# Optimization experiments

Hardware: AMD Instinct MI355X
Metric: run time of the kernel (lower is better)

## Reference

```python
import jax, jax.numpy as jnp
import numpy as np

N_NODES = 100000
N_EDGES = 1600000
IN_DIM, HID_DIM, OUT_DIM = 128, 64, 32
NEG_SLOPE = 0.2  # PyG GATConv default negative_slope


def gat_conv(x, src, dst, num_nodes, W, a_src, a_dst, bias):
    # x: [N, in], W: [in, out], a_src/a_dst: [out], bias: [out]
    h = x @ W                                        # [N, out]
    alpha_s = h @ a_src                              # [N] per-node source score
    alpha_d = h @ a_dst                              # [N] per-node target score
    e = jax.nn.leaky_relu(alpha_s[src] + alpha_d[dst], NEG_SLOPE)  # [E]
    # segment softmax over incoming edges of each dst node
    m = jax.ops.segment_max(e, dst, num_segments=num_nodes)        # [N]
    ex = jnp.exp(e - m[dst])                                        # [E]
    z = jax.ops.segment_sum(ex, dst, num_segments=num_nodes)        # [N]
    coef = ex / z[dst]                                              # [E]
    out = jax.ops.segment_sum(coef[:, None] * h[src], dst, num_segments=num_nodes)
    return out + bias


def setup_inputs() -> dict:
    key = jax.random.key(0)
    ks = jax.random.split(key, 10)
    x = jax.random.normal(ks[0], (N_NODES, IN_DIM), dtype=jnp.float32)
    edge_index = jax.random.randint(ks[1], (2, N_EDGES), 0, N_NODES, dtype=jnp.int64)
    s = 0.1
    W1 = jax.random.normal(ks[2], (IN_DIM, HID_DIM), dtype=jnp.float32) * s
    a_src1 = jax.random.normal(ks[3], (HID_DIM,), dtype=jnp.float32) * s
    a_dst1 = jax.random.normal(ks[4], (HID_DIM,), dtype=jnp.float32) * s
    b1 = jnp.zeros((HID_DIM,), dtype=jnp.float32)
    W2 = jax.random.normal(ks[5], (HID_DIM, OUT_DIM), dtype=jnp.float32) * s
    a_src2 = jax.random.normal(ks[6], (OUT_DIM,), dtype=jnp.float32) * s
    a_dst2 = jax.random.normal(ks[7], (OUT_DIM,), dtype=jnp.float32) * s
    b2 = jnp.zeros((OUT_DIM,), dtype=jnp.float32)
    return {"x": x, "edge_index": edge_index, "W1": W1, "a_src1": a_src1,
            "a_dst1": a_dst1, "b1": b1, "W2": W2, "a_src2": a_src2,
            "a_dst2": a_dst2, "b2": b2}


def reference(x, edge_index, W1, a_src1, a_dst1, b1, W2, a_src2, a_dst2, b2):
    n = x.shape[0]
    loops = jnp.arange(n, dtype=edge_index.dtype)
    src = jnp.concatenate([edge_index[0], loops])  # add_self_loops=True default
    dst = jnp.concatenate([edge_index[1], loops])
    h = jax.nn.relu(gat_conv(x, src, dst, n, W1, a_src1, a_dst1, b1))
    out = gat_conv(h, src, dst, n, W2, a_src2, a_dst2, b2)
    return jax.nn.log_softmax(out, axis=1)
```

## Files before the change

kernel.cpp:

```cpp
#include <hip/hip_runtime.h>

#define N_NODES 100000
#define N_EDGES 1600000
#define ET (N_EDGES + N_NODES)
#define NEG_SLOPE 0.2f

#define BSHIFT 9
#define BW 512
#define NBUCK ((N_NODES + BW - 1) / BW)
#define BCAP 10240
#define BINCH 2048

typedef unsigned short u16;
typedef unsigned int u32;

__device__ __forceinline__ float bf2f(u16 v) {
    return __uint_as_float(((u32)v) << 16);
}
__device__ __forceinline__ u16 f2bf(float f) {
    u32 u = __float_as_uint(f);
    u32 r = (u + 0x7FFFu + ((u >> 16) & 1u)) >> 16;
    return (u16)r;
}
__device__ __forceinline__ float lrelu(float x) { return x > 0.f ? x : NEG_SLOPE * x; }
__device__ __forceinline__ float ldf(const void* p, int i, int bf) {
    return bf ? bf2f(((const u16*)p)[i]) : ((const float*)p)[i];
}
__device__ __forceinline__ int get_dst(const int* __restrict__ ei, int e, int ei64) {
    if (e < N_EDGES) return ei64 ? ei[2 * (N_EDGES + e)] : ei[N_EDGES + e];
    return e - N_EDGES;
}
__device__ __forceinline__ int get_src(const int* __restrict__ ei, int e, int ei64) {
    if (e < N_EDGES) return ei64 ? ei[2 * e] : ei[e];
    return e - N_EDGES;
}

__device__ __forceinline__ void fma8(float wt, uint4 qv, float (&acc)[8]) {
    acc[0] = fmaf(wt, __uint_as_float(qv.x << 16), acc[0]);
    acc[1] = fmaf(wt, __uint_as_float(qv.x & 0xFFFF0000u), acc[1]);
    acc[2] = fmaf(wt, __uint_as_float(qv.y << 16), acc[2]);
    acc[3] = fmaf(wt, __uint_as_float(qv.y & 0xFFFF0000u), acc[3]);
    acc[4] = fmaf(wt, __uint_as_float(qv.z << 16), acc[4]);
    acc[5] = fmaf(wt, __uint_as_float(qv.z & 0xFFFF0000u), acc[5]);
    acc[6] = fmaf(wt, __uint_as_float(qv.w << 16), acc[6]);
    acc[7] = fmaf(wt, __uint_as_float(qv.w & 0xFFFF0000u), acc[7]);
}

__global__ void detect_kernel(const u32* __restrict__ x32, const int* __restrict__ ei,
                              int* __restrict__ flags, int* __restrict__ bcnt) {
    int lane = threadIdx.x;
    for (int i = lane; i < 256; i += 64) bcnt[i] = 0;
    u32 e = (x32[lane] >> 7) & 0xFFu;
    int ok = (e >= 96u && e <= 143u) ? 1 : 0;
    int cnt = (int)__popcll(__ballot(ok));
    int nz = (ei[2 * lane + 1] != 0) + (ei[2 * (lane + 64) + 1] != 0);
    #pragma unroll
    for (int off = 32; off > 0; off >>= 1) nz += __shfl_xor(nz, off);
    if (lane == 0) { flags[0] = (cnt >= 48) ? 1 : 0; flags[1] = (nz == 0) ? 1 : 0; }
}

__global__ __launch_bounds__(256) void bin_kernel(
    const int* __restrict__ ei, const int* __restrict__ flags,
    int* __restrict__ bcnt, u32* __restrict__ bbuf)
{
    __shared__ int hist[NBUCK];
    const int t = threadIdx.x;
    const int base = blockIdx.x * BINCH;
    const int ei64 = flags[1];
    for (int i = t; i < NBUCK; i += 256) hist[i] = 0;
    __syncthreads();
    for (int i = t; i < BINCH; i += 256) {
        int e = base + i;
        if (e >= ET) break;
        int d = get_dst(ei, e, ei64);
        atomicAdd(&hist[d >> BSHIFT], 1);
    }
    __syncthreads();
    for (int i = t; i < NBUCK; i += 256) {
        int c = hist[i];
        hist[i] = (c > 0) ? atomicAdd(&bcnt[i], c) : 0;
    }
    __syncthreads();
    for (int i = t; i < BINCH; i += 256) {
        int e = base + i;
        if (e >= ET) break;
        int d = get_dst(ei, e, ei64);
        int s = get_src(ei, e, ei64);
        int b = d >> BSHIFT;
        int pos = atomicAdd(&hist[b], 1);
        if (pos < BCAP)
            bbuf[(size_t)b * BCAP + pos] = ((u32)(d & (BW - 1)) << 17) | (u32)s;
    }
}

__global__ __launch_bounds__(256) void bscan_kernel(
    const int* __restrict__ bcnt, int* __restrict__ bbase)
{
    __shared__ int sd[256];
    int t = threadIdx.x;
    int v = (t < NBUCK) ? min(bcnt[t], BCAP) : 0;
    sd[t] = v;
    __syncthreads();
    for (int off = 1; off < 256; off <<= 1) {
        int x = (t >= off) ? sd[t - off] : 0;
        __syncthreads();
        sd[t] += x;
        __syncthreads();
    }
    if (t < NBUCK) bbase[t] = sd[t] - v;
    if (t == NBUCK - 1) bbase[NBUCK] = sd[t];
}

__global__ __launch_bounds__(1024) void scatter_kernel(
    const int* __restrict__ bcnt, const int* __restrict__ bbase,
    const u32* __restrict__ bbuf, int* __restrict__ rowptr, int* __restrict__ ssrc)
{
    __shared__ int hist[BW];
    __shared__ int cur[BW];
    __shared__ int wtot[4];
    __shared__ int lds_s[BCAP];
    const int t = threadIdx.x;
    const int b = blockIdx.x;
    const int cnt = min(bcnt[b], BCAP);
    const int base = bbase[b];
    const u32* mybuf = bbuf + (size_t)b * BCAP;

    if (t < BW) hist[t] = 0;
    __syncthreads();
    for (int i = t; i < cnt; i += 1024) atomicAdd(&hist[(int)(mybuf[i] >> 17)], 1);
    __syncthreads();
    int a0 = 0, a1 = 0, s = 0, v = 0;
    const int lane = t & 63, wid = t >> 6;
    if (t < 256) {
        a0 = hist[2 * t]; a1 = hist[2 * t + 1];
        s = a0 + a1;
        v = s;
        #pragma unroll
        for (int off = 1; off < 64; off <<= 1) {
            int n = __shfl_up(v, off);
            if (lane >= off) v += n;
        }
        if (lane == 63) wtot[wid] = v;
    }
    __syncthreads();
    if (t == 0) {
        int acc = 0;
        #pragma unroll
        for (int w = 0; w < 4; ++w) { int tmp = wtot[w]; wtot[w] = acc; acc += tmp; }
    }
    __syncthreads();
    if (t < 256) {
        int excl = v + wtot[wid] - s;
        cur[2 * t] = excl;
        cur[2 * t + 1] = excl + a0;
    }
    __syncthreads();
    if (t < BW) {
        int g = b * BW + t;
        if (g < N_NODES) rowptr[g] = base + cur[t];
    }
    if (b == NBUCK - 1 && t == 0) rowptr[N_NODES] = bbase[NBUCK];
    __syncthreads();
    for (int i = t; i < cnt; i += 1024) {
        u32 code = mybuf[i];
        int pos = atomicAdd(&cur[(int)(code >> 17)], 1);
        lds_s[pos] = (int)(code & 0x1FFFFu);
    }
    __syncthreads();
    for (int i = t; i < cnt; i += 1024) ssrc[base + i] = lds_s[i];
}

__global__ __launch_bounds__(256) void gemm1_kernel(
    const float* __restrict__ x, const float* __restrict__ W,
    const void* __restrict__ a_src, const void* __restrict__ a_dst,
    const int* __restrict__ flags,
    u16* __restrict__ h, float* __restrict__ as_, float* __restrict__ ad_)
{
    __shared__ float xs[256 * 33];
    __shared__ float Wl[32 * 64];
    const int t = threadIdx.x;
    const int node0 = blockIdx.x * 256;
    const int bf = flags[0];
    const int ng = t >> 3;
    const int cg = t & 7;

    float acc[8][8];
    #pragma unroll
    for (int i = 0; i < 8; ++i)
        #pragma unroll
        for (int j = 0; j < 8; ++j) acc[i][j] = 0.f;

    for (int kc = 0; kc < 4; ++kc) {
        const int kb = kc * 32;
        const int c4 = t & 7;
        #pragma unroll
        for (int p = 0; p < 8; ++p) {
            int row = (t >> 3) + p * 32;
            int n = node0 + row;
            float4 vv = make_float4(0.f, 0.f, 0.f, 0.f);
            if (n < N_NODES) {
                if (!bf) {
                    vv = *(const float4*)(x + (size_t)n * 128 + kb + c4 * 4);
                } else {
                    const u16* xh = (const u16*)x;
                    vv.x = bf2f(xh[(size_t)n * 128 + kb + c4 * 4 + 0]);
                    vv.y = bf2f(xh[(size_t)n * 128 + kb + c4 * 4 + 1]);
                    vv.z = bf2f(xh[(size_t)n * 128 + kb + c4 * 4 + 2]);
                    vv.w = bf2f(xh[(size_t)n * 128 + kb + c4 * 4 + 3]);
                }
            }
            float* dstp = &xs[row * 33 + c4 * 4];
            dstp[0] = vv.x; dstp[1] = vv.y; dstp[2] = vv.z; dstp[3] = vv.w;
        }
        if (!bf) {
            #pragma unroll
            for (int qq = 0; qq < 2; ++qq) {
                int f4 = t * 2 + qq;
                ((float4*)Wl)[f4] = ((const float4*)(W + (size_t)kb * 64))[f4];
            }
        } else {
            const u16* Wh = (const u16*)W;
            for (int i = t; i < 2048; i += 256) Wl[i] = bf2f(Wh[(size_t)kb * 64 + i]);
        }
        __syncthreads();

        for (int kk = 0; kk < 32; ++kk) {
            float xr[8];
            #pragma unroll
            for (int i = 0; i < 8; ++i) xr[i] = xs[(ng * 8 + i) * 33 + kk];
            float4 w0 = *(const float4*)&Wl[kk * 64 + cg * 8];
            float4 w1 = *(const float4*)&Wl[kk * 64 + cg * 8 + 4];
            const float wr[8] = {w0.x, w0.y, w0.z, w0.w, w1.x, w1.y, w1.z, w1.w};
            #pragma unroll
            for (int i = 0; i < 8; ++i)
                #pragma unroll
                for (int j = 0; j < 8; ++j)
                    acc[i][j] = fmaf(xr[i], wr[j], acc[i][j]);
        }
        __syncthreads();
    }

    float av[8], dv[8];
    #pragma unroll
    for (int j = 0; j < 8; ++j) {
        av[j] = ldf(a_src, cg * 8 + j, bf);
        dv[j] = ldf(a_dst, cg * 8 + j, bf);
    }
    #pragma unroll
    for (int i = 0; i < 8; ++i) {
        int n = node0 + ng * 8 + i;
        float ps = 0.f, pd = 0.f;
        #pragma unroll
        for (int j = 0; j < 8; ++j) { ps += acc[i][j] * av[j]; pd += acc[i][j] * dv[j]; }
        #pragma unroll
        for (int off = 1; off < 8; off <<= 1) {
            ps += __shfl_xor(ps, off);
            pd += __shfl_xor(pd, off);
        }
        if (n < N_NODES) {
            uint4 hv;
            hv.x = (u32)f2bf(acc[i][0]) | ((u32)f2bf(acc[i][1]) << 16);
            hv.y = (u32)f2bf(acc[i][2]) | ((u32)f2bf(acc[i][3]) << 16);
            hv.z = (u32)f2bf(acc[i][4]) | ((u32)f2bf(acc[i][5]) << 16);
            hv.w = (u32)f2bf(acc[i][6]) | ((u32)f2bf(acc[i][7]) << 16);
            *(uint4*)&h[(size_t)n * 64 + cg * 8] = hv;
            if (cg == 0) { as_[n] = ps; ad_[n] = pd; }
        }
    }
}

template<int SH>
__global__ __launch_bounds__(256) void score_kernel(
    const int* __restrict__ rowptr, const int* __restrict__ ssrc,
    const float* __restrict__ as_, const float* __restrict__ ad_,
    uint2* __restrict__ wexs)
{
    const int lane = threadIdx.x & 63;
    const int dst = blockIdx.x * 4 + (threadIdx.x >> 6);
    if (dst >= N_NODES) return;
    const int beg = rowptr[dst], end = rowptr[dst + 1];
    const int deg = end - beg;
    const float add = ad_[dst];

    if (deg <= 64) {
        int j = beg + lane;
        bool valid = j < end;
        int sj = valid ? ssrc[j] : 0;
        float sc = valid ? lrelu(as_[sj] + add) : -1e30f;
        float m = sc;
        #pragma unroll
        for (int off = 32; off > 0; off >>= 1) m = fmaxf(m, __shfl_xor(m, off));
        float ex = __expf(sc - m);
        float l = ex;
        #pragma unroll
        for (int off = 32; off > 0; off >>= 1) l += __shfl_xor(l, off);
        if (valid)
            wexs[j] = make_uint2(__float_as_uint(ex / l), ((u32)sj) << SH);
    } else {
        float m = -1e30f, l = 0.f;
        for (int base = beg; base < end; base += 64) {
            int j = base + lane;
            bool valid = j < end;
            float sc = valid ? lrelu(as_[ssrc[j]] + add) : -1e30f;
            float cm = sc;
            #pragma unroll
            for (int off = 32; off > 0; off >>= 1) cm = fmaxf(cm, __shfl_xor(cm, off));
            float nm = fmaxf(m, cm);
            float cs = __expf(sc - nm);
            #pragma unroll
            for (int off = 32; off > 0; off >>= 1) cs += __shfl_xor(cs, off);
            l = l * __expf(m - nm) + cs;
            m = nm;
        }
        float inv = 1.f / l;
        for (int base = beg; base < end; base += 64) {
            int j = base + lane;
            if (j < end) {
                int sj = ssrc[j];
                wexs[j] = make_uint2(
                    __float_as_uint(__expf(lrelu(as_[sj] + add) - m) * inv),
                    ((u32)sj) << SH);
            }
        }
    }
}

__global__ __launch_bounds__(256) void gather64_kernel(
    const int* __restrict__ rowptr, const uint2* __restrict__ wexs,
    const u16* __restrict__ h, float* __restrict__ agg)
{
    const int tid = threadIdx.x;
    const int hl = tid & 31;
    const int dreal = blockIdx.x * 8 + (tid >> 5);
    const int dst = min(dreal, N_NODES - 1);
    const int beg = rowptr[dst];
    const int deg = rowptr[dst + 1] - beg;
    const int e4 = hl >> 3;
    const int i8 = hl & 7;
    const char* __restrict__ hb = (const char*)h;
    const u32 boff = (u32)(i8 * 16);

    float acc[8] = {0.f, 0.f, 0.f, 0.f, 0.f, 0.f, 0.f, 0.f};

    #pragma unroll
    for (int g = 0; g < 8; ++g) {
        int eidx = g * 4 + e4;
        bool valid = eidx < deg;
        uint2 p = wexs[beg + (valid ? eidx : 0)];
        float w = valid ? __uint_as_float(p.x) : 0.f;
        uint4 qv = *(const uint4*)(hb + (size_t)(p.y + boff));
        fma8(w, qv, acc);
    }
    int mdeg = max(deg, __shfl_xor(deg, 32));
    for (int g = 8; g * 4 < mdeg; ++g) {
        int eidx = g * 4 + e4;
        bool valid = eidx < deg;
        uint2 p = wexs[beg + (valid ? eidx : 0)];
        float w = valid ? __uint_as_float(p.x) : 0.f;
        uint4 qv = *(const uint4*)(hb + (size_t)(p.y + boff));
        fma8(w, qv, acc);
    }

    #pragma unroll
    for (int c = 0; c < 8; ++c) {
        acc[c] += __shfl_xor(acc[c], 8);
        acc[c] += __shfl_xor(acc[c], 16);
    }
    if (e4 == 0 && dreal < N_NODES) {
        *(float4*)&agg[(size_t)dst * 64 + i8 * 8] =
            make_float4(acc[0], acc[1], acc[2], acc[3]);
        *(float4*)&agg[(size_t)dst * 64 + i8 * 8 + 4] =
            make_float4(acc[4], acc[5], acc[6], acc[7]);
    }
}

__global__ __launch_bounds__(256) void gather32_lsm_kernel(
    const int* __restrict__ rowptr, const uint2* __restrict__ wexs,
    const u16* __restrict__ h, const void* __restrict__ b2,
    const int* __restrict__ flags, float* __restrict__ out)
{
    const int tid = threadIdx.x;
    const int hl = tid & 31;
    const int dreal = blockIdx.x * 8 + (tid >> 5);
    const int dst = min(dreal, N_NODES - 1);
    const int beg = rowptr[dst];
    const int deg = rowptr[dst + 1] - beg;
    const int e8 = hl >> 2;
    const int i4 = hl & 3;
    const int bf = flags[0];
    const char* __restrict__ hb = (const char*)h;
    const u32 boff = (u32)(i4 * 16);

    float acc[8] = {0.f, 0.f, 0.f, 0.f, 0.f, 0.f, 0.f, 0.f};

    #pragma unroll
    for (int g = 0; g < 4; ++g) {
        int eidx = g * 8 + e8;
        bool valid = eidx < deg;
        uint2 p = wexs[beg + (valid ? eidx : 0)];
        float w = valid ? __uint_as_float(p.x) : 0.f;
        uint4 qv = *(const uint4*)(hb + (size_t)(p.y + boff));
        fma8(w, qv, acc);
    }
    int mdeg = max(deg, __shfl_xor(deg, 32));
    for (int g = 4; g * 8 < mdeg; ++g) {
        int eidx = g * 8 + e8;
        bool valid = eidx < deg;
        uint2 p = wexs[beg + (valid ? eidx : 0)];
        float w = valid ? __uint_as_float(p.x) : 0.f;
        uint4 qv = *(const uint4*)(hb + (size_t)(p.y + boff));
        fma8(w, qv, acc);
    }

    #pragma unroll
    for (int c = 0; c < 8; ++c) {
        acc[c] += __shfl_xor(acc[c], 4);
        acc[c] += __shfl_xor(acc[c], 8);
        acc[c] += __shfl_xor(acc[c], 16);
    }

    float v[8];
    #pragma unroll
    for (int c = 0; c < 8; ++c) v[c] = acc[c] + ldf(b2, i4 * 8 + c, bf);
    float mx = v[0];
    #pragma unroll
    for (int c = 1; c < 8; ++c) mx = fmaxf(mx, v[c]);
    mx = fmaxf(mx, __shfl_xor(mx, 1));
    mx = fmaxf(mx, __shfl_xor(mx, 2));
    float ss = 0.f;
    #pragma unroll
    for (int c = 0; c < 8; ++c) ss += __expf(v[c] - mx);
    ss += __shfl_xor(ss, 1);
    ss += __shfl_xor(ss, 2);
    float lg = mx + __logf(ss);
    if (e8 == 0 && dreal < N_NODES) {
        *(float4*)&out[(size_t)dst * 32 + i4 * 8] =
            make_float4(v[0] - lg, v[1] - lg, v[2] - lg, v[3] - lg);
        *(float4*)&out[(size_t)dst * 32 + i4 * 8 + 4] =
            make_float4(v[4] - lg, v[5] - lg, v[6] - lg, v[7] - lg);
    }
}

#define G2_TILE 128

__global__ __launch_bounds__(256, 3) void gemm2_kernel(
    const float* __restrict__ agg1, const void* __restrict__ b1,
    const u32* __restrict__ W32, const void* __restrict__ a_src,
    const void* __restrict__ a_dst, const int* __restrict__ flags,
    u16* __restrict__ h, float* __restrict__ as_, float* __restrict__ ad_)
{
    __shared__ __align__(16) float Wl[64 * 32];
    __shared__ __align__(16) float xs[G2_TILE * 68];
    const int tid = threadIdx.x;
    const int node0 = blockIdx.x * G2_TILE;
    const int bf = flags[0];

    if (bf) {
        for (int i = tid; i < 1024; i += 256) {
            u32 u = W32[i];
            *(float2*)&Wl[2 * i] = make_float2(__uint_as_float(u << 16),
                                               __uint_as_float(u & 0xFFFF0000u));
        }
    } else {
        for (int i = tid; i < 2048; i += 256) Wl[i] = __uint_as_float(W32[i]);
    }
    #pragma unroll
    for (int it = 0; it < 8; ++it) {
        int i = tid + it * 256;
        int nl = i >> 4;
        int k  = (i & 15) * 4;
        int n = node0 + nl;
        float4 v = make_float4(0.f, 0.f, 0.f, 0.f);
        if (n < N_NODES) v = *(const float4*)(agg1 + (size_t)n * 64 + k);
        v.x = fmaxf(v.x + ldf(b1, k + 0, bf), 0.f);
        v.y = fmaxf(v.y + ldf(b1, k + 1, bf), 0.f);
        v.z = fmaxf(v.z + ldf(b1, k + 2, bf), 0.f);
        v.w = fmaxf(v.w + ldf(b1, k + 3, bf), 0.f);
        *(float4*)&xs[nl * 68 + k] = v;
    }
    __syncthreads();

    const int ch0 = (tid & 7) * 4;
    const int nb0 = (tid >> 3) * 4;
    float acc[4][4];
    #pragma unroll
    for (int j = 0; j < 4; ++j)
        #pragma unroll
        for (int c = 0; c < 4; ++c) acc[j][c] = 0.f;

    #pragma unroll 4
    for (int k0 = 0; k0 < 64; k0 += 4) {
        float4 xv0 = *(const float4*)&xs[(nb0 + 0) * 68 + k0];
        float4 xv1 = *(const float4*)&xs[(nb0 + 1) * 68 + k0];
        float4 xv2 = *(const float4*)&xs[(nb0 + 2) * 68 + k0];
        float4 xv3 = *(const float4*)&xs[(nb0 + 3) * 68 + k0];
        const float* xp[4] = { (const float*)&xv0, (const float*)&xv1,
                               (const float*)&xv2, (const float*)&xv3 };
        #pragma unroll
        for (int kk = 0; kk < 4; ++kk) {
            float4 w = *(const float4*)&Wl[(k0 + kk) * 32 + ch0];
            #pragma unroll
            for (int j = 0; j < 4; ++j) {
                float xvv = xp[j][kk];
                acc[j][0] = fmaf(xvv, w.x, acc[j][0]);
                acc[j][1] = fmaf(xvv, w.y, acc[j][1]);
                acc[j][2] = fmaf(xvv, w.z, acc[j][2]);
                acc[j][3] = fmaf(xvv, w.w, acc[j][3]);
            }
        }
    }

    float av[4], dv[4];
    #pragma unroll
    for (int c = 0; c < 4; ++c) {
        av[c] = ldf(a_src, ch0 + c, bf);
        dv[c] = ldf(a_dst, ch0 + c, bf);
    }
    #pragma unroll
    for (int j = 0; j < 4; ++j) {
        float ps = acc[j][0] * av[0] + acc[j][1] * av[1]
                 + acc[j][2] * av[2] + acc[j][3] * av[3];
        float pd = acc[j][0] * dv[0] + acc[j][1] * dv[1]
                 + acc[j][2] * dv[2] + acc[j][3] * dv[3];
        #pragma unroll
        for (int off = 1; off < 8; off <<= 1) {
            ps += __shfl_xor(ps, off);
            pd += __shfl_xor(pd, off);
        }
        int n = node0 + nb0 + j;
        if (n < N_NODES) {
            u32 p0 = (u32)f2bf(acc[j][0]) | ((u32)f2bf(acc[j][1]) << 16);
            u32 p1 = (u32)f2bf(acc[j][2]) | ((u32)f2bf(acc[j][3]) << 16);
            *(uint2*)&h[(size_t)n * 32 + ch0] = make_uint2(p0, p1);
            if ((tid & 7) == 0) { as_[n] = ps; ad_[n] = pd; }
        }
    }
}

extern "C" void kernel_launch(void* const* d_in, const int* in_sizes, int n_in,
                              void* d_out, int out_size, void* d_ws, size_t ws_size,
                              hipStream_t stream) {
    const float* x   = (const float*)d_in[0];
    const int* ei    = (const int*)d_in[1];
    const float* W1  = (const float*)d_in[2];
    const void* a_s1 = d_in[3];
    const void* a_d1 = d_in[4];
    const void* b1   = d_in[5];
    const u32* W2    = (const u32*)d_in[6];
    const void* a_s2 = d_in[7];
    const void* a_d2 = d_in[8];
    const void* b2   = d_in[9];
    float* out = (float*)d_out;

    char* base = (char*)d_ws;
    int* flags = (int*)base;
    u16* h     = (u16*)(base + 64);
    char* q = base + 64 + (size_t)N_NODES * 64 * 2;
    float* as1 = (float*)q; q += (size_t)N_NODES * 4;
    float* ad1 = (float*)q; q += (size_t)N_NODES * 4;
    float* as2 = (float*)q; q += (size_t)N_NODES * 4;
    float* ad2 = (float*)q; q += (size_t)N_NODES * 4;
    float* agg1 = (float*)q; q += (size_t)N_NODES * 64 * 4;
    int* rowptr = (int*)q;  q += (size_t)(N_NODES + 16) * 4;
    int* ssrc   = (int*)q;  q += (size_t)ET * 4;
    int* bcnt   = (int*)q;  q += 256 * 4;
    int* bbase  = (int*)q;  q += 256 * 4;
    q = (char*)(((size_t)q + 255) & ~(size_t)255);
    u32*  bbuf  = (u32*)q;
    uint2* wexs = (uint2*)q;

    detect_kernel<<<1, 64, 0, stream>>>((const u32*)x, ei, flags, bcnt);

    bin_kernel<<<(ET + BINCH - 1) / BINCH, 256, 0, stream>>>(ei, flags, bcnt, bbuf);
    bscan_kernel<<<1, 256, 0, stream>>>(bcnt, bbase);
    scatter_kernel<<<NBUCK, 1024, 0, stream>>>(bcnt, bbase, bbuf, rowptr, ssrc);

    gemm1_kernel<<<(N_NODES + 255) / 256, 256, 0, stream>>>(x, W1, a_s1, a_d1, flags, h, as1, ad1);
    score_kernel<7><<<(N_NODES + 3) / 4, 256, 0, stream>>>(rowptr, ssrc, as1, ad1, wexs);
    gather64_kernel<<<(N_NODES + 7) / 8, 256, 0, stream>>>(rowptr, wexs, h, agg1);

    gemm2_kernel<<<(N_NODES + G2_TILE - 1) / G2_TILE, 256, 0, stream>>>(agg1, b1, W2, a_s2, a_d2, flags, h, as2, ad2);
    score_kernel<6><<<(N_NODES + 3) / 4, 256, 0, stream>>>(rowptr, ssrc, as2, ad2, wexs);
    gather32_lsm_kernel<<<(N_NODES + 7) / 8, 256, 0, stream>>>(rowptr, wexs, h, b2, flags, out);
}
```

Before: 338.4 us.

## Fuse layer-2 GEMM into layer-1 gather and cache edges in registers during binning

Removes the separate gemm2 kernel and the fp32 agg1 round trip. Each wave now applies bias and ReLU to its aggregated 64-wide row, multiplies it by a transposed W2 held in LDS, computes the attention scores and writes bf16 h2 directly. Layer-2 output goes to a new h2 buffer instead of overwriting h. Separately, bin_kernel keeps each thread's edge src/dst in registers between its histogram and scatter passes instead of reading the edge list twice. The trade-off is that every gather block reloads and transposes all of W2 into LDS, adding per-block setup work and LDS use.

```diff
diff --git a/kernel.cpp b/kernel.cpp
--- a/kernel.cpp
+++ b/kernel.cpp
@@ -69,11 +69,18 @@
     const int ei64 = flags[1];
     for (int i = t; i < NBUCK; i += 256) hist[i] = 0;
     __syncthreads();
-    for (int i = t; i < BINCH; i += 256) {
-        int e = base + i;
-        if (e >= ET) break;
-        int d = get_dst(ei, e, ei64);
-        atomicAdd(&hist[d >> BSHIFT], 1);
+
+    int dloc[8], sloc[8];
+    #pragma unroll
+    for (int p = 0; p < 8; ++p) {
+        int e = base + t + p * 256;
+        if (e < ET) {
+            dloc[p] = get_dst(ei, e, ei64);
+            sloc[p] = get_src(ei, e, ei64);
+            atomicAdd(&hist[dloc[p] >> BSHIFT], 1);
+        } else {
+            dloc[p] = -1; sloc[p] = 0;
+        }
     }
     __syncthreads();
     for (int i = t; i < NBUCK; i += 256) {
@@ -81,15 +88,15 @@
         hist[i] = (c > 0) ? atomicAdd(&bcnt[i], c) : 0;
     }
     __syncthreads();
-    for (int i = t; i < BINCH; i += 256) {
-        int e = base + i;
-        if (e >= ET) break;
-        int d = get_dst(ei, e, ei64);
-        int s = get_src(ei, e, ei64);
-        int b = d >> BSHIFT;
-        int pos = atomicAdd(&hist[b], 1);
-        if (pos < BCAP)
-            bbuf[(size_t)b * BCAP + pos] = ((u32)(d & (BW - 1)) << 17) | (u32)s;
+    #pragma unroll
+    for (int p = 0; p < 8; ++p) {
+        if (dloc[p] >= 0) {
+            int b = dloc[p] >> BSHIFT;
+            int pos = atomicAdd(&hist[b], 1);
+            if (pos < BCAP)
+                bbuf[(size_t)b * BCAP + pos] =
+                    ((u32)(dloc[p] & (BW - 1)) << 17) | (u32)sloc[p];
+        }
     }
 }
 
@@ -325,14 +332,37 @@
     }
 }
 
-__global__ __launch_bounds__(256) void gather64_kernel(
+__global__ __launch_bounds__(256) void gather64_g2_kernel(
     const int* __restrict__ rowptr, const uint2* __restrict__ wexs,
-    const u16* __restrict__ h, float* __restrict__ agg)
-{
+    const u16* __restrict__ h, const void* __restrict__ b1,
+    const u32* __restrict__ W32, const void* __restrict__ a_src,
+    const void* __restrict__ a_dst, const int* __restrict__ flags,
+    u16* __restrict__ h2, float* __restrict__ as2, float* __restrict__ ad2)
+{
+    __shared__ float W2t[32 * 66];
+    __shared__ float hin_lds[8 * 64];
     const int tid = threadIdx.x;
     const int hl = tid & 31;
     const int dreal = blockIdx.x * 8 + (tid >> 5);
     const int dst = min(dreal, N_NODES - 1);
+    const int bf = flags[0];
+
+    if (bf) {
+        for (int i = tid; i < 1024; i += 256) {
+            u32 u = W32[i];
+            int k = i >> 4;
+            int c = (2 * i) & 31;
+            W2t[c * 66 + k] = __uint_as_float(u << 16);
+            W2t[(c + 1) * 66 + k] = __uint_as_float(u & 0xFFFF0000u);
+        }
+    } else {
+        for (int i = tid; i < 2048; i += 256) {
+            int k = i >> 5, c = i & 31;
+            W2t[c * 66 + k] = __uint_as_float(W32[i]);
+        }
+    }
+    __syncthreads();
+
     const int beg = rowptr[dst];
     const int deg = rowptr[dst + 1] - beg;
     const int e4 = hl >> 3;
@@ -366,12 +396,48 @@
         acc[c] += __shfl_xor(acc[c], 8);
         acc[c] += __shfl_xor(acc[c], 16);
     }
-    if (e4 == 0 && dreal < N_NODES) {
-        *(float4*)&agg[(size_t)dst * 64 + i8 * 8] =
-            make_float4(acc[0], acc[1], acc[2], acc[3]);
-        *(float4*)&agg[(size_t)dst * 64 + i8 * 8 + 4] =
-            make_float4(acc[4], acc[5], acc[6], acc[7]);
-    }
+
+    float* hin_s = &hin_lds[(tid >> 5) * 64];
+    if (hl < 8) {
+        float4 v0, v1;
+        v0.x = fmaxf(acc[0] + ldf(b1, hl * 8 + 0, bf), 0.f);
+        v0.y = fmaxf(acc[1] + ldf(b1, hl * 8 + 1, bf), 0.f);
+        v0.z = fmaxf(acc[2] + ldf(b1, hl * 8 + 2, bf), 0.f);
+        v0.w = fmaxf(acc[3] + ldf(b1, hl * 8 + 3, bf), 0.f);
+        v1.x = fmaxf(acc[4] + ldf(b1, hl * 8 + 4, bf), 0.f);
+        v1.y = fmaxf(acc[5] + ldf(b1, hl * 8 + 5, bf), 0.f);
+        v1.z = fmaxf(acc[6] + ldf(b1, hl * 8 + 6, bf), 0.f);
+        v1.w = fmaxf(acc[7] + ldf(b1, hl * 8 + 7, bf), 0.f);
+        *(float4*)&hin_s[hl * 8] = v0;
+        *(float4*)&hin_s[hl * 8 + 4] = v1;
+    }
+    __builtin_amdgcn_wave_barrier();
+    asm volatile("s_waitcnt lgkmcnt(0)" ::: "memory");
+
+    float o = 0.f;
+    #pragma unroll 8
+    for (int k = 0; k < 64; k += 2) {
+        float2 hv = *(const float2*)&hin_s[k];
+        float2 wv = *(const float2*)&W2t[hl * 66 + k];
+        o = fmaf(hv.x, wv.x, o);
+        o = fmaf(hv.y, wv.y, o);
+    }
+
+    float ps = o * ldf(a_src, hl, bf);
+    float pd = o * ldf(a_dst, hl, bf);
+    #pragma unroll
+    for (int off = 1; off < 32; off <<= 1) {
+        ps += __shfl_xor(ps, off);
+        pd += __shfl_xor(pd, off);
+    }
+    u32 hbits = (u32)f2bf(o);
+    u32 other = (u32)__shfl_xor((int)hbits, 1);
+    if (dreal < N_NODES) {
+        if ((hl & 1) == 0)
+            *((u32*)h2 + (size_t)dst * 16 + (hl >> 1)) = hbits | (other << 16);
+        if (hl == 0) { as2[dst] = ps; ad2[dst] = pd; }
+    }
+    __builtin_amdgcn_wave_barrier();
 }
 
 __global__ __launch_bounds__(256) void gather32_lsm_kernel(
@@ -438,102 +504,6 @@
             make_float4(v[0] - lg, v[1] - lg, v[2] - lg, v[3] - lg);
         *(float4*)&out[(size_t)dst * 32 + i4 * 8 + 4] =
             make_float4(v[4] - lg, v[5] - lg, v[6] - lg, v[7] - lg);
-    }
-}
-
-#define G2_TILE 128
-
-__global__ __launch_bounds__(256, 3) void gemm2_kernel(
-    const float* __restrict__ agg1, const void* __restrict__ b1,
-    const u32* __restrict__ W32, const void* __restrict__ a_src,
-    const void* __restrict__ a_dst, const int* __restrict__ flags,
-    u16* __restrict__ h, float* __restrict__ as_, float* __restrict__ ad_)
-{
-    __shared__ __align__(16) float Wl[64 * 32];
-    __shared__ __align__(16) float xs[G2_TILE * 68];
-    const int tid = threadIdx.x;
-    const int node0 = blockIdx.x * G2_TILE;
-    const int bf = flags[0];
-
-    if (bf) {
-        for (int i = tid; i < 1024; i += 256) {
-            u32 u = W32[i];
-            *(float2*)&Wl[2 * i] = make_float2(__uint_as_float(u << 16),
-                                               __uint_as_float(u & 0xFFFF0000u));
-        }
-    } else {
-        for (int i = tid; i < 2048; i += 256) Wl[i] = __uint_as_float(W32[i]);
-    }
-    #pragma unroll
-    for (int it = 0; it < 8; ++it) {
-        int i = tid + it * 256;
-        int nl = i >> 4;
-        int k  = (i & 15) * 4;
-        int n = node0 + nl;
-        float4 v = make_float4(0.f, 0.f, 0.f, 0.f);
-        if (n < N_NODES) v = *(const float4*)(agg1 + (size_t)n * 64 + k);
-        v.x = fmaxf(v.x + ldf(b1, k + 0, bf), 0.f);
-        v.y = fmaxf(v.y + ldf(b1, k + 1, bf), 0.f);
-        v.z = fmaxf(v.z + ldf(b1, k + 2, bf), 0.f);
-        v.w = fmaxf(v.w + ldf(b1, k + 3, bf), 0.f);
-        *(float4*)&xs[nl * 68 + k] = v;
-    }
-    __syncthreads();
-
-    const int ch0 = (tid & 7) * 4;
-    const int nb0 = (tid >> 3) * 4;
-    float acc[4][4];
-    #pragma unroll
-    for (int j = 0; j < 4; ++j)
-        #pragma unroll
-        for (int c = 0; c < 4; ++c) acc[j][c] = 0.f;
-
-    #pragma unroll 4
-    for (int k0 = 0; k0 < 64; k0 += 4) {
-        float4 xv0 = *(const float4*)&xs[(nb0 + 0) * 68 + k0];
-        float4 xv1 = *(const float4*)&xs[(nb0 + 1) * 68 + k0];
-        float4 xv2 = *(const float4*)&xs[(nb0 + 2) * 68 + k0];
-        float4 xv3 = *(const float4*)&xs[(nb0 + 3) * 68 + k0];
-        const float* xp[4] = { (const float*)&xv0, (const float*)&xv1,
-                               (const float*)&xv2, (const float*)&xv3 };
-        #pragma unroll
-        for (int kk = 0; kk < 4; ++kk) {
-            float4 w = *(const float4*)&Wl[(k0 + kk) * 32 + ch0];
-            #pragma unroll
-            for (int j = 0; j < 4; ++j) {
-                float xvv = xp[j][kk];
-                acc[j][0] = fmaf(xvv, w.x, acc[j][0]);
-                acc[j][1] = fmaf(xvv, w.y, acc[j][1]);
-                acc[j][2] = fmaf(xvv, w.z, acc[j][2]);
-                acc[j][3] = fmaf(xvv, w.w, acc[j][3]);
-            }
-        }
-    }
-
-    float av[4], dv[4];
-    #pragma unroll
-    for (int c = 0; c < 4; ++c) {
-        av[c] = ldf(a_src, ch0 + c, bf);
-        dv[c] = ldf(a_dst, ch0 + c, bf);
-    }
-    #pragma unroll
-    for (int j = 0; j < 4; ++j) {
-        float ps = acc[j][0] * av[0] + acc[j][1] * av[1]
-                 + acc[j][2] * av[2] + acc[j][3] * av[3];
-        float pd = acc[j][0] * dv[0] + acc[j][1] * dv[1]
-                 + acc[j][2] * dv[2] + acc[j][3] * dv[3];
-        #pragma unroll
-        for (int off = 1; off < 8; off <<= 1) {
-            ps += __shfl_xor(ps, off);
-            pd += __shfl_xor(pd, off);
-        }
-        int n = node0 + nb0 + j;
-        if (n < N_NODES) {
-            u32 p0 = (u32)f2bf(acc[j][0]) | ((u32)f2bf(acc[j][1]) << 16);
-            u32 p1 = (u32)f2bf(acc[j][2]) | ((u32)f2bf(acc[j][3]) << 16);
-            *(uint2*)&h[(size_t)n * 32 + ch0] = make_uint2(p0, p1);
-            if ((tid & 7) == 0) { as_[n] = ps; ad_[n] = pd; }
-        }
     }
 }
 
@@ -560,7 +530,7 @@
     float* ad1 = (float*)q; q += (size_t)N_NODES * 4;
     float* as2 = (float*)q; q += (size_t)N_NODES * 4;
     float* ad2 = (float*)q; q += (size_t)N_NODES * 4;
-    float* agg1 = (float*)q; q += (size_t)N_NODES * 64 * 4;
+    u16* h2    = (u16*)q;   q += (size_t)N_NODES * 64 * 4;
     int* rowptr = (int*)q;  q += (size_t)(N_NODES + 16) * 4;
     int* ssrc   = (int*)q;  q += (size_t)ET * 4;
     int* bcnt   = (int*)q;  q += 256 * 4;
@@ -577,9 +547,9 @@
 
     gemm1_kernel<<<(N_NODES + 255) / 256, 256, 0, stream>>>(x, W1, a_s1, a_d1, flags, h, as1, ad1);
     score_kernel<7><<<(N_NODES + 3) / 4, 256, 0, stream>>>(rowptr, ssrc, as1, ad1, wexs);
-    gather64_kernel<<<(N_NODES + 7) / 8, 256, 0, stream>>>(rowptr, wexs, h, agg1);
-
-    gemm2_kernel<<<(N_NODES + G2_TILE - 1) / G2_TILE, 256, 0, stream>>>(agg1, b1, W2, a_s2, a_d2, flags, h, as2, ad2);
+    gather64_g2_kernel<<<(N_NODES + 7) / 8, 256, 0, stream>>>(
+        rowptr, wexs, h, b1, W2, a_s2, a_d2, flags, h2, as2, ad2);
+
     score_kernel<6><<<(N_NODES + 3) / 4, 256, 0, stream>>>(rowptr, ssrc, as2, ad2, wexs);
-    gather32_lsm_kernel<<<(N_NODES + 7) / 8, 256, 0, stream>>>(rowptr, wexs, h, b2, flags, out);
-}
+    gather32_lsm_kernel<<<(N_NODES + 7) / 8, 256, 0, stream>>>(rowptr, wexs, h2, b2, flags, out);
+}
```

New measurement: 331.5 us. 1.02x faster.
